# Kernel optimization log

Measured on AMD Instinct MI355X. Metric: run time of the kernel, lower is better.

## Reference

```python
import jax, jax.numpy as jnp
import numpy as np

B, T, C = 4, 2048, 1024
H = 16
D = C // H  # head_dim = 64


def setup_inputs() -> dict:
    key = jax.random.key(0)
    ks = jax.random.split(key, 11)
    s = 0.02
    return {
        "q": jax.random.normal(ks[0], (B, T, C), jnp.float32),
        "k": jax.random.normal(ks[1], (B, T, C), jnp.float32),
        "v": jax.random.normal(ks[2], (B, T, C), jnp.float32),
        "Wq": jax.random.normal(ks[3], (C, C), jnp.float32) * s,
        "bq": jnp.zeros((C,), jnp.float32),
        "Wk": jax.random.normal(ks[4], (C, C), jnp.float32) * s,
        "bk": jnp.zeros((C,), jnp.float32),
        "Wv": jax.random.normal(ks[5], (C, C), jnp.float32) * s,
        "bv": jnp.zeros((C,), jnp.float32),
        "Wo": jax.random.normal(ks[6], (C, C), jnp.float32) * s,
        "bo": jnp.zeros((C,), jnp.float32),
    }


def reference(q, k, v, Wq, bq, Wk, bk, Wv, bv, Wo, bo):
    # projections (torch Linear: x @ W.T + b)
    qh = (q @ Wq.T + bq).reshape(B, T, H, D).transpose(0, 2, 1, 3)  # [B,H,T,D]
    kh = (k @ Wk.T + bk).reshape(B, T, H, D).transpose(0, 2, 1, 3)
    vh = (v @ Wv.T + bv).reshape(B, T, H, D).transpose(0, 2, 1, 3)
    scores = jnp.einsum('bhqd,bhkd->bhqk', qh, kh) * (D ** -0.5)  # [B,H,T,T]
    # causal mask (is_causal=True)
    causal = jnp.tril(jnp.ones((T, T), bool))
    scores = jnp.where(causal, scores, -jnp.inf)
    probs = jax.nn.softmax(scores, axis=-1)
    # dropout_rate=0.0 -> identity in eval mode
    out = jnp.einsum('bhqk,bhkd->bhqd', probs, vh)  # [B,H,T,D]
    out = out.transpose(0, 2, 1, 3).reshape(B, T, C)
    return out @ Wo.T + bo
```

## Files before the change

### kernel.cpp

```cpp
#include <hip/hip_runtime.h>
#include <hip/hip_bf16.h>

typedef __attribute__((ext_vector_type(8))) short bf16x8;
typedef __attribute__((ext_vector_type(4))) float f32x4;
typedef __attribute__((ext_vector_type(16))) float f32x16;

__device__ __forceinline__ unsigned short f2bf(float x) {
  union { float f; unsigned u; } v; v.f = x;
  unsigned r = v.u + 0x7fffu + ((v.u >> 16) & 1u);
  return (unsigned short)(r >> 16);
}

__device__ __forceinline__ unsigned cvtpk_bf16(float lo, float hi) {
  unsigned r;
  asm("v_cvt_pk_bf16_f32 %0, %1, %2" : "=v"(r) : "v"(lo), "v"(hi));
  return r;
}
__device__ __forceinline__ void pl32swap(unsigned &a, unsigned &b) {
  asm volatile("v_permlane32_swap_b32 %0, %1" : "+v"(a), "+v"(b));
}
__device__ __forceinline__ void gload_lds16(const void* g, void* l) {
  __builtin_amdgcn_global_load_lds((const __attribute__((address_space(1))) void*)g,
                                   (__attribute__((address_space(3))) void*)l, 16, 0, 0);
}

#define SWZ(x) ((x) ^ ((((x) >> 7) & 7) << 4))

__global__ __launch_bounds__(256) void cvt_w(
    const float* __restrict__ W0, const float* __restrict__ W1,
    const float* __restrict__ W2, const float* __restrict__ W3,
    unsigned short* __restrict__ o0, unsigned short* __restrict__ o1,
    unsigned short* __restrict__ o2, unsigned short* __restrict__ o3,
    float s0) {
  const int z = blockIdx.y;
  const float* W = (z == 0) ? W0 : (z == 1) ? W1 : (z == 2) ? W2 : W3;
  unsigned short* o = (z == 0) ? o0 : (z == 1) ? o1 : (z == 2) ? o2 : o3;
  const float s = (z == 0) ? s0 : 1.0f;
  const int i = blockIdx.x * 256 + threadIdx.x;
  const float4 x = ((const float4*)W)[i];
  uint2 u;
  u.x = cvtpk_bf16(x.x * s, x.y * s);
  u.y = cvtpk_bf16(x.z * s, x.w * s);
  ((uint2*)o)[i] = u;
}


__global__ __launch_bounds__(256) void proj_gemm3(
    const float* __restrict__ A0, const float* __restrict__ A1, const float* __restrict__ A2,
    const unsigned short* __restrict__ W0b, const unsigned short* __restrict__ W1b,
    const unsigned short* __restrict__ W2b,
    const float* __restrict__ b0, const float* __restrict__ b1, const float* __restrict__ b2,
    unsigned short* __restrict__ o0, unsigned short* __restrict__ o1,
    unsigned short* __restrict__ o2) {
  const int K = 1024;
  const int NK = 32;
  __shared__ __align__(16) unsigned short As[3][4096];
  __shared__ __align__(16) unsigned short Bs[3][4096];
  const int z = blockIdx.z;
  const float* A = (z == 0) ? A0 : (z == 1) ? A1 : A2;
  const unsigned short* Wb = (z == 0) ? W0b : (z == 1) ? W1b : W2b;
  const float* bias = (z == 0) ? b0 : (z == 1) ? b1 : b2;
  unsigned short* out = (z == 0) ? o0 : (z == 1) ? o1 : o2;
  const float bscale = (z == 0) ? 0.125f * 1.4426950408889634f : 1.0f;
  const int vtrans = (z == 2);

  const int tid = threadIdx.x;
  const int row0 = blockIdx.x * 128;
  const int col0 = blockIdx.y * 128;
  const int lane = tid & 63;
  const int w = tid >> 6;
  const int wm = (w >> 1) * 64, wn = (w & 1) * 64;
  const int fr = lane & 15;
  const int g = lane >> 4;
  const int frh = fr >> 1;
  const int gcf = ((fr & 1) * 4 + g) ^ frh;
  const int aoff = wm * 64 + frh * 128 + gcf * 16;
  const int boff = wn * 64 + frh * 128 + gcf * 16;

  const int ar = tid >> 2;
  const int acq = tid & 3;
  const float* asrc0 = &A[(size_t)(row0 + ar) * K + acq * 8];
  const float* asrc1 = asrc0 + (size_t)64 * K;
  const int awr = (ar >> 1) * 128 + ((((ar & 1) * 4 + acq) ^ ((ar >> 1) & 7)) * 16);

  const unsigned short* bsrc[2];
  int bldso[2];
#pragma unroll
  for (int j = 0; j < 2; ++j) {
    const int L = (w * 2 + j) * 64 + lane;
    const int pp = L >> 3, gc = L & 7;
    const int e = gc ^ (pp & 7);
    const int r = pp * 2 + (e >> 2), c = e & 3;
    bsrc[j] = Wb + (size_t)(col0 + r) * K + c * 8;
    bldso[j] = (w * 2 + j) * 1024;
  }

  f32x4 acc[4][4] = {};
  float4 la0[4], la1[4];

#define LOADA(kt, LA)                                        \
  {                                                          \
    const float* s0_ = asrc0 + (kt) * 32;                    \
    const float* s1_ = asrc1 + (kt) * 32;                    \
    LA[0] = *(const float4*)s0_; LA[1] = *(const float4*)(s0_ + 4); \
    LA[2] = *(const float4*)s1_; LA[3] = *(const float4*)(s1_ + 4); \
  }
#define STOREA(buf, LA)                                               \
  {                                                                   \
    uint4 u0_, u1_;                                                   \
    u0_.x = cvtpk_bf16(LA[0].x, LA[0].y); u0_.y = cvtpk_bf16(LA[0].z, LA[0].w); \
    u0_.z = cvtpk_bf16(LA[1].x, LA[1].y); u0_.w = cvtpk_bf16(LA[1].z, LA[1].w); \
    u1_.x = cvtpk_bf16(LA[2].x, LA[2].y); u1_.y = cvtpk_bf16(LA[2].z, LA[2].w); \
    u1_.z = cvtpk_bf16(LA[3].x, LA[3].y); u1_.w = cvtpk_bf16(LA[3].z, LA[3].w); \
    char* base_ = (char*)As[buf];                                     \
    *(uint4*)(base_ + awr) = u0_;                                     \
    *(uint4*)(base_ + awr + 4096) = u1_;                              \
  }
#define STAGEB(buf, kt)                                               \
  {                                                                   \
    gload_lds16(bsrc[0] + (kt) * 32, (char*)Bs[buf] + bldso[0]);      \
    gload_lds16(bsrc[1] + (kt) * 32, (char*)Bs[buf] + bldso[1]);      \
  }
#define COMPUTE(cb)                                                   \
  {                                                                   \
    const char* Ab_ = (const char*)As[cb];                            \
    const char* Bb_ = (const char*)Bs[cb];                            \
    bf16x8 af[4], bfv[4];                                             \
    _Pragma("unroll")                                                 \
    for (int i = 0; i < 4; ++i) {                                     \
      af[i] = *(const bf16x8*)(Ab_ + aoff + i * 1024);                \
      bfv[i] = *(const bf16x8*)(Bb_ + boff + i * 1024);               \
    }                                                                 \
    _Pragma("unroll")                                                 \
    for (int i = 0; i < 4; ++i)                                       \
      _Pragma("unroll")                                               \
      for (int j = 0; j < 4; ++j)                                     \
        acc[i][j] = __builtin_amdgcn_mfma_f32_16x16x32_bf16(af[i], bfv[j], acc[i][j], 0, 0, 0); \
  }

  STAGEB(0, 0); STAGEB(1, 1);
  LOADA(0, la0); LOADA(1, la1);
  STOREA(0, la0);
  asm volatile("s_waitcnt lgkmcnt(0)" ::: "memory");

  int cur = 0;
  for (int kt = 0; kt < NK; kt += 2) {
    if (kt == 0) asm volatile("s_waitcnt vmcnt(0)" ::: "memory");
    else         asm volatile("s_waitcnt vmcnt(6)" ::: "memory");
    __builtin_amdgcn_sched_barrier(0);
    __builtin_amdgcn_s_barrier();
    __builtin_amdgcn_sched_barrier(0);
    {
      const int nx1 = (cur == 2) ? 0 : cur + 1;
      const int nx2 = (nx1 == 2) ? 0 : nx1 + 1;
      if (kt + 2 < NK) { LOADA(kt + 2, la0); STAGEB(nx2, kt + 2); }
      __builtin_amdgcn_sched_barrier(0);
      COMPUTE(cur);
      STOREA(nx1, la1);
      asm volatile("s_waitcnt lgkmcnt(0)" ::: "memory");
      cur = nx1;
    }
    if (kt + 1 == NK - 1) asm volatile("s_waitcnt vmcnt(0)" ::: "memory");
    else                  asm volatile("s_waitcnt vmcnt(6)" ::: "memory");
    __builtin_amdgcn_sched_barrier(0);
    __builtin_amdgcn_s_barrier();
    __builtin_amdgcn_sched_barrier(0);
    {
      const int nx1 = (cur == 2) ? 0 : cur + 1;
      const int nx2 = (nx1 == 2) ? 0 : nx1 + 1;
      if (kt + 3 < NK) { LOADA(kt + 3, la1); STAGEB(nx2, kt + 3); }
      __builtin_amdgcn_sched_barrier(0);
      COMPUTE(cur);
      if (kt + 2 < NK) {
        STOREA(nx1, la0);
        asm volatile("s_waitcnt lgkmcnt(0)" ::: "memory");
      }
      cur = nx1;
    }
  }
#undef LOADA
#undef STOREA
#undef STAGEB
#undef COMPUTE

#pragma unroll
  for (int j = 0; j < 4; ++j) {
    const int n = col0 + wn + j * 16 + fr;
    const float bv = bias[n] * bscale;
    const int h = n >> 6, d = n & 63;
#pragma unroll
    for (int i = 0; i < 4; ++i) {
      const int mrow = row0 + wm + i * 16 + g * 4;
      const int b = mrow >> 11, t0 = mrow & 2047;
      if (vtrans) {
        uint2 u;
        u.x = cvtpk_bf16(acc[i][j][0] + bv, acc[i][j][1] + bv);
        u.y = cvtpk_bf16(acc[i][j][2] + bv, acc[i][j][3] + bv);
        *(uint2*)(&out[(((size_t)b * 16 + h) * 64 + d) * 2048 + t0]) = u;
      } else {
#pragma unroll
        for (int r = 0; r < 4; ++r)
          out[(((size_t)b * 16 + h) * 2048 + (t0 + r)) * 64 + d] = f2bf(acc[i][j][r] + bv);
      }
    }
  }
}

__global__ __launch_bounds__(256) void out_gemm(
    const unsigned short* __restrict__ A, const unsigned short* __restrict__ Wb,
    const float* __restrict__ bias, float* __restrict__ out) {
  const int K = 1024;
  const int NK = 32;
  __shared__ __align__(16) unsigned short As[3][4096];
  __shared__ __align__(16) unsigned short Bs[3][4096];
  const int tid = threadIdx.x;
  const int row0 = blockIdx.x * 128;
  const int col0 = blockIdx.y * 128;
  const int lane = tid & 63;
  const int w = tid >> 6;
  const int wm = (w >> 1) * 64, wn = (w & 1) * 64;
  const int fr = lane & 15;
  const int g = lane >> 4;
  const int frh = fr >> 1;
  const int gcf = ((fr & 1) * 4 + g) ^ frh;
  const int aoff = wm * 64 + frh * 128 + gcf * 16;
  const int boff = wn * 64 + frh * 128 + gcf * 16;

  const unsigned short* asrc[2];
  const unsigned short* bsrc[2];
  int ldso[2];
#pragma unroll
  for (int j = 0; j < 2; ++j) {
    const int L = (w * 2 + j) * 64 + lane;
    const int pp = L >> 3, gc = L & 7;
    const int e = gc ^ (pp & 7);
    const int r = pp * 2 + (e >> 2), c = e & 3;
    asrc[j] = A + (size_t)(row0 + r) * K + c * 8;
    bsrc[j] = Wb + (size_t)(col0 + r) * K + c * 8;
    ldso[j] = (w * 2 + j) * 1024;
  }

  f32x4 acc[4][4] = {};

  auto stage = [&](int buf, int kt) {
#pragma unroll
    for (int j = 0; j < 2; ++j) {
      gload_lds16(asrc[j] + kt * 32, (char*)As[buf] + ldso[j]);
      gload_lds16(bsrc[j] + kt * 32, (char*)Bs[buf] + ldso[j]);
    }
  };

  stage(0, 0); stage(1, 1);
  int cur = 0;
  for (int kt = 0; kt < NK; ++kt) {
    if (kt == 0 || kt == NK - 1) asm volatile("s_waitcnt vmcnt(0)" ::: "memory");
    else                         asm volatile("s_waitcnt vmcnt(4)" ::: "memory");
    __builtin_amdgcn_sched_barrier(0);
    __builtin_amdgcn_s_barrier();
    __builtin_amdgcn_sched_barrier(0);
    const int nx1 = (cur == 2) ? 0 : cur + 1;
    const int nx2 = (nx1 == 2) ? 0 : nx1 + 1;
    if (kt + 2 < NK) stage(nx2, kt + 2);
    __builtin_amdgcn_sched_barrier(0);
    const char* Ab = (const char*)As[cur];
    const char* Bb = (const char*)Bs[cur];
    bf16x8 af[4], bfv[4];
#pragma unroll
    for (int i = 0; i < 4; ++i) {
      af[i] = *(const bf16x8*)(Ab + aoff + i * 1024);
      bfv[i] = *(const bf16x8*)(Bb + boff + i * 1024);
    }
#pragma unroll
    for (int i = 0; i < 4; ++i)
#pragma unroll
      for (int j = 0; j < 4; ++j)
        acc[i][j] = __builtin_amdgcn_mfma_f32_16x16x32_bf16(af[i], bfv[j], acc[i][j], 0, 0, 0);
    cur = nx1;
  }

#pragma unroll
  for (int j = 0; j < 4; ++j) {
    const int n = col0 + wn + j * 16 + fr;
    const float bv = bias[n];
#pragma unroll
    for (int i = 0; i < 4; ++i) {
      const int mrow = row0 + wm + i * 16 + g * 4;
#pragma unroll
      for (int r = 0; r < 4; ++r)
        out[(size_t)(mrow + r) * 1024 + n] = acc[i][j][r] + bv;
    }
  }
}

__global__ __launch_bounds__(256) void attn_mfma(
    const unsigned short* __restrict__ qh, const unsigned short* __restrict__ kh,
    const unsigned short* __restrict__ vT, unsigned short* __restrict__ Ob) {
  __shared__ __align__(16) unsigned short Klds[2][64 * 64];
  __shared__ __align__(16) unsigned short Vlds[2][64 * 64];

  const int tid = threadIdx.x;
  const int lane = tid & 63;
  const int w = tid >> 6;
  const int bh = blockIdx.y;
  const int b = bh >> 4, h = bh & 15;
  const int q32 = lane & 31;
  const int hi = lane >> 5;

  const char* kbase = (const char*)(kh + (size_t)bh * 2048 * 64);
  const char* vbase = (const char*)(vT + (size_t)bh * 64 * 2048);

  const int lrow = lane >> 3;
  const int cb = (((lane & 7) ^ lrow) << 4);

  auto stage = [&](int buf, int t) {
    const int kv0 = t * 64;
#pragma unroll
    for (int j = 0; j < 2; ++j) {
      const int c = w * 2 + j;
      const int r = c * 8 + lrow;
      gload_lds16(kbase + (size_t)(kv0 + r) * 128 + cb,
                  (char*)Klds[buf] + c * 1024);
      gload_lds16(vbase + (size_t)r * 4096 + (size_t)kv0 * 2 + cb,
                  (char*)Vlds[buf] + c * 1024);
    }
  };

  for (int pass = 0; pass < 2; ++pass) {
    const int qt = pass == 0 ? (15 - (int)blockIdx.x) : (int)blockIdx.x;
    const int qb = qt * 128 + w * 32;
    const int nt = 2 * qt + 2;

    bf16x8 qf[4];
    {
      const unsigned short* qp = qh + ((size_t)bh * 2048 + qb + q32) * 64;
#pragma unroll
      for (int kk = 0; kk < 4; ++kk)
        qf[kk] = *(const bf16x8*)(qp + kk * 16 + hi * 8);
    }

    f32x16 acc_o[2] = {};
    float m_run = -INFINITY, l_run = 0.f;

    stage(0, 0);
    __syncthreads();

    int cur = 0;
    for (int t = 0; t < nt; ++t) {
      const int kv0 = t * 64;
      if (t + 1 < nt) stage(cur ^ 1, t + 1);

      if (kv0 < qb + 32) {
        const char* Kb = (const char*)Klds[cur];
        const char* Vb = (const char*)Vlds[cur];

        f32x16 sacc[2] = {};
        __builtin_amdgcn_s_setprio(1);
#pragma unroll
        for (int kk = 0; kk < 4; ++kk) {
          bf16x8 kf0 = *(const bf16x8*)(Kb + SWZ((q32) * 128 + kk * 32 + hi * 16));
          bf16x8 kf1 = *(const bf16x8*)(Kb + SWZ((32 + q32) * 128 + kk * 32 + hi * 16));
          sacc[0] = __builtin_amdgcn_mfma_f32_32x32x16_bf16(kf0, qf[kk], sacc[0], 0, 0, 0);
          sacc[1] = __builtin_amdgcn_mfma_f32_32x32x16_bf16(kf1, qf[kk], sacc[1], 0, 0, 0);
        }
        __builtin_amdgcn_s_setprio(0);

        if (kv0 + 64 > qb) {
          const int qa = qb + q32;
#pragma unroll
          for (int mkv = 0; mkv < 2; ++mkv)
#pragma unroll
            for (int r = 0; r < 16; ++r) {
              const int kva = kv0 + mkv * 32 + 4 * hi + (r & 3) + 8 * (r >> 2);
              if (kva > qa) sacc[mkv][r] = -INFINITY;
            }
        }

        float mx = -INFINITY;
#pragma unroll
        for (int mkv = 0; mkv < 2; ++mkv)
#pragma unroll
          for (int r = 0; r < 16; ++r) mx = fmaxf(mx, sacc[mkv][r]);
        mx = fmaxf(mx, __shfl_xor(mx, 32));
        if (!__all(mx <= m_run + 8.f)) {
          const float mnew = fmaxf(m_run, mx);
          const float al = exp2f(m_run - mnew);
          m_run = mnew;
          l_run *= al;
          acc_o[0] = acc_o[0] * al;
          acc_o[1] = acc_o[1] * al;
        }

        float ls = 0.f;
        unsigned W[2][8];
#pragma unroll
        for (int mkv = 0; mkv < 2; ++mkv)
#pragma unroll
          for (int s = 0; s < 8; ++s) {
            const float p0 = exp2f(sacc[mkv][2 * s] - m_run);
            const float p1 = exp2f(sacc[mkv][2 * s + 1] - m_run);
            ls += p0 + p1;
            W[mkv][s] = cvtpk_bf16(p0, p1);
          }
        ls += __shfl_xor(ls, 32);
        l_run += ls;

#pragma unroll
        for (int mkv = 0; mkv < 2; ++mkv) {
          pl32swap(W[mkv][0], W[mkv][2]);
          pl32swap(W[mkv][1], W[mkv][3]);
          pl32swap(W[mkv][4], W[mkv][6]);
          pl32swap(W[mkv][5], W[mkv][7]);
        }

        __builtin_amdgcn_s_setprio(1);
#pragma unroll
        for (int wg = 0; wg < 4; ++wg) {
          union { unsigned u[4]; bf16x8 v; } pk;
          pk.u[0] = W[wg >> 1][(wg & 1) * 4 + 0];
          pk.u[1] = W[wg >> 1][(wg & 1) * 4 + 1];
          pk.u[2] = W[wg >> 1][(wg & 1) * 4 + 2];
          pk.u[3] = W[wg >> 1][(wg & 1) * 4 + 3];
          bf16x8 vf0 = *(const bf16x8*)(Vb + SWZ((q32) * 128 + wg * 32 + hi * 16));
          bf16x8 vf1 = *(const bf16x8*)(Vb + SWZ((32 + q32) * 128 + wg * 32 + hi * 16));
          acc_o[0] = __builtin_amdgcn_mfma_f32_32x32x16_bf16(vf0, pk.v, acc_o[0], 0, 0, 0);
          acc_o[1] = __builtin_amdgcn_mfma_f32_32x32x16_bf16(vf1, pk.v, acc_o[1], 0, 0, 0);
        }
        __builtin_amdgcn_s_setprio(0);
      }

      __syncthreads();
      cur ^= 1;
    }

    {
      const float inv = 1.0f / l_run;
      const int qa = qb + q32;
      unsigned short* op = Ob + ((size_t)b * 2048 + qa) * 1024 + h * 64;
#pragma unroll
      for (int md = 0; md < 2; ++md)
#pragma unroll
        for (int rr = 0; rr < 4; ++rr) {
          uint2 u;
          u.x = cvtpk_bf16(acc_o[md][rr * 4 + 0] * inv, acc_o[md][rr * 4 + 1] * inv);
          u.y = cvtpk_bf16(acc_o[md][rr * 4 + 2] * inv, acc_o[md][rr * 4 + 3] * inv);
          *(uint2*)(op + md * 32 + rr * 8 + hi * 4) = u;
        }
    }
  }
}

extern "C" void kernel_launch(void* const* d_in, const int* in_sizes, int n_in,
                              void* d_out, int out_size, void* d_ws, size_t ws_size,
                              hipStream_t stream) {
  (void)in_sizes; (void)n_in; (void)out_size; (void)ws_size;
  const float* q = (const float*)d_in[0];
  const float* k = (const float*)d_in[1];
  const float* v = (const float*)d_in[2];
  const float* Wq = (const float*)d_in[3];
  const float* bq = (const float*)d_in[4];
  const float* Wk = (const float*)d_in[5];
  const float* bk = (const float*)d_in[6];
  const float* Wv = (const float*)d_in[7];
  const float* bv = (const float*)d_in[8];
  const float* Wo = (const float*)d_in[9];
  const float* bo = (const float*)d_in[10];
  float* out = (float*)d_out;

  const size_t SZ = (size_t)4 * 16 * 2048 * 64;
  const size_t WSZ = (size_t)1024 * 1024;
  unsigned short* qh = (unsigned short*)d_ws;
  unsigned short* kh = qh + SZ;
  unsigned short* vT = kh + SZ;
  unsigned short* Ob = vT + SZ;
  unsigned short* Wqb = Ob + SZ;
  unsigned short* Wkb = Wqb + WSZ;
  unsigned short* Wvb = Wkb + WSZ;
  unsigned short* Wob = Wvb + WSZ;

  dim3 g0(1024, 4), b0(256);
  cvt_w<<<g0, b0, 0, stream>>>(Wq, Wk, Wv, Wo, Wqb, Wkb, Wvb, Wob,
                               0.125f * 1.4426950408889634f);

  dim3 g1(64, 8, 3), b1(256);
  proj_gemm3<<<g1, b1, 0, stream>>>(q, k, v, Wqb, Wkb, Wvb, bq, bk, bv, qh, kh, vT);

  dim3 g2(8, 64), b2(256);
  attn_mfma<<<g2, b2, 0, stream>>>(qh, kh, vT, Ob);

  dim3 g3(64, 8), b3(256);
  out_gemm<<<g3, b3, 0, stream>>>(Ob, Wob, bo, out);
}
```

Before: 201.2 us.

## Load activation operand straight to registers, stage only weights in LDS

```diff
diff --git a/kernel.cpp b/kernel.cpp
--- a/kernel.cpp
+++ b/kernel.cpp
@@ -54,10 +54,9 @@
     unsigned short* __restrict__ o2) {
   const int K = 1024;
   const int NK = 32;
-  __shared__ __align__(16) unsigned short As[3][4096];
-  __shared__ __align__(16) unsigned short Bs[3][4096];
+  __shared__ __align__(16) unsigned short Ws[3][4096];
   const int z = blockIdx.z;
-  const float* A = (z == 0) ? A0 : (z == 1) ? A1 : A2;
+  const float* X = (z == 0) ? A0 : (z == 1) ? A1 : A2;
   const unsigned short* Wb = (z == 0) ? W0b : (z == 1) ? W1b : W2b;
   const float* bias = (z == 0) ? b0 : (z == 1) ? b1 : b2;
   unsigned short* out = (z == 0) ? o0 : (z == 1) ? o1 : o2;
@@ -65,229 +64,257 @@
   const int vtrans = (z == 2);
 
   const int tid = threadIdx.x;
-  const int row0 = blockIdx.x * 128;
-  const int col0 = blockIdx.y * 128;
+  const int m0 = blockIdx.x * 128;
+  const int n0 = blockIdx.y * 128;
   const int lane = tid & 63;
   const int w = tid >> 6;
-  const int wm = (w >> 1) * 64, wn = (w & 1) * 64;
+  const int wnA = (w >> 1) * 64;
+  const int wmB = (w & 1) * 64;
   const int fr = lane & 15;
   const int g = lane >> 4;
   const int frh = fr >> 1;
   const int gcf = ((fr & 1) * 4 + g) ^ frh;
-  const int aoff = wm * 64 + frh * 128 + gcf * 16;
-  const int boff = wn * 64 + frh * 128 + gcf * 16;
-
-  const int ar = tid >> 2;
-  const int acq = tid & 3;
-  const float* asrc0 = &A[(size_t)(row0 + ar) * K + acq * 8];
-  const float* asrc1 = asrc0 + (size_t)64 * K;
-  const int awr = (ar >> 1) * 128 + ((((ar & 1) * 4 + acq) ^ ((ar >> 1) & 7)) * 16);
-
-  const unsigned short* bsrc[2];
-  int bldso[2];
+  const int aoff = wnA * 64 + frh * 128 + gcf * 16;
+
+  const unsigned short* wsrc[2];
+  int wldo[2];
 #pragma unroll
   for (int j = 0; j < 2; ++j) {
     const int L = (w * 2 + j) * 64 + lane;
     const int pp = L >> 3, gc = L & 7;
     const int e = gc ^ (pp & 7);
     const int r = pp * 2 + (e >> 2), c = e & 3;
-    bsrc[j] = Wb + (size_t)(col0 + r) * K + c * 8;
-    bldso[j] = (w * 2 + j) * 1024;
-  }
+    wsrc[j] = Wb + (size_t)(n0 + r) * K + c * 8;
+    wldo[j] = (w * 2 + j) * 1024;
+  }
+
+  const float* xsrc[4];
+#pragma unroll
+  for (int j = 0; j < 4; ++j)
+    xsrc[j] = X + (size_t)(m0 + wmB + j * 16 + fr) * K + g * 8;
 
   f32x4 acc[4][4] = {};
-  float4 la0[4], la1[4];
-
-#define LOADA(kt, LA)                                        \
-  {                                                          \
-    const float* s0_ = asrc0 + (kt) * 32;                    \
-    const float* s1_ = asrc1 + (kt) * 32;                    \
-    LA[0] = *(const float4*)s0_; LA[1] = *(const float4*)(s0_ + 4); \
-    LA[2] = *(const float4*)s1_; LA[3] = *(const float4*)(s1_ + 4); \
-  }
-#define STOREA(buf, LA)                                               \
+  float4 laA[8], laB[8];
+
+#define LOADX(kt, LA)                                                 \
   {                                                                   \
-    uint4 u0_, u1_;                                                   \
-    u0_.x = cvtpk_bf16(LA[0].x, LA[0].y); u0_.y = cvtpk_bf16(LA[0].z, LA[0].w); \
-    u0_.z = cvtpk_bf16(LA[1].x, LA[1].y); u0_.w = cvtpk_bf16(LA[1].z, LA[1].w); \
-    u1_.x = cvtpk_bf16(LA[2].x, LA[2].y); u1_.y = cvtpk_bf16(LA[2].z, LA[2].w); \
-    u1_.z = cvtpk_bf16(LA[3].x, LA[3].y); u1_.w = cvtpk_bf16(LA[3].z, LA[3].w); \
-    char* base_ = (char*)As[buf];                                     \
-    *(uint4*)(base_ + awr) = u0_;                                     \
-    *(uint4*)(base_ + awr + 4096) = u1_;                              \
-  }
-#define STAGEB(buf, kt)                                               \
+    _Pragma("unroll")                                                 \
+    for (int j = 0; j < 4; ++j) {                                     \
+      LA[j * 2 + 0] = *(const float4*)(xsrc[j] + (kt) * 32);          \
+      LA[j * 2 + 1] = *(const float4*)(xsrc[j] + (kt) * 32 + 4);      \
+    }                                                                 \
+  }
+#define STAGEW(buf, kt)                                               \
   {                                                                   \
-    gload_lds16(bsrc[0] + (kt) * 32, (char*)Bs[buf] + bldso[0]);      \
-    gload_lds16(bsrc[1] + (kt) * 32, (char*)Bs[buf] + bldso[1]);      \
-  }
-#define COMPUTE(cb)                                                   \
+    gload_lds16(wsrc[0] + (kt) * 32, (char*)Ws[buf] + wldo[0]);       \
+    gload_lds16(wsrc[1] + (kt) * 32, (char*)Ws[buf] + wldo[1]);       \
+  }
+#define COMPUTE(cb, LA)                                               \
   {                                                                   \
-    const char* Ab_ = (const char*)As[cb];                            \
-    const char* Bb_ = (const char*)Bs[cb];                            \
-    bf16x8 af[4], bfv[4];                                             \
-    _Pragma("unroll")                                                 \
-    for (int i = 0; i < 4; ++i) {                                     \
-      af[i] = *(const bf16x8*)(Ab_ + aoff + i * 1024);                \
-      bfv[i] = *(const bf16x8*)(Bb_ + boff + i * 1024);               \
+    union { unsigned u[4]; bf16x8 v; } xf[4];                         \
+    _Pragma("unroll")                                                 \
+    for (int j = 0; j < 4; ++j) {                                     \
+      xf[j].u[0] = cvtpk_bf16(LA[j * 2 + 0].x, LA[j * 2 + 0].y);      \
+      xf[j].u[1] = cvtpk_bf16(LA[j * 2 + 0].z, LA[j * 2 + 0].w);      \
+      xf[j].u[2] = cvtpk_bf16(LA[j * 2 + 1].x, LA[j * 2 + 1].y);      \
+      xf[j].u[3] = cvtpk_bf16(LA[j * 2 + 1].z, LA[j * 2 + 1].w);      \
     }                                                                 \
+    const char* Ab_ = (const char*)Ws[cb];                            \
+    bf16x8 af[4];                                                     \
+    _Pragma("unroll")                                                 \
+    for (int i = 0; i < 4; ++i) af[i] = *(const bf16x8*)(Ab_ + aoff + i * 1024); \
     _Pragma("unroll")                                                 \
     for (int i = 0; i < 4; ++i)                                       \
       _Pragma("unroll")                                               \
       for (int j = 0; j < 4; ++j)                                     \
-        acc[i][j] = __builtin_amdgcn_mfma_f32_16x16x32_bf16(af[i], bfv[j], acc[i][j], 0, 0, 0); \
-  }
-
-  STAGEB(0, 0); STAGEB(1, 1);
-  LOADA(0, la0); LOADA(1, la1);
-  STOREA(0, la0);
-  asm volatile("s_waitcnt lgkmcnt(0)" ::: "memory");
+        acc[i][j] = __builtin_amdgcn_mfma_f32_16x16x32_bf16(af[i], xf[j].v, acc[i][j], 0, 0, 0); \
+  }
+
+  LOADX(0, laA);
+  __builtin_amdgcn_sched_barrier(0);
+  STAGEW(0, 0); STAGEW(1, 1);
+  __builtin_amdgcn_sched_barrier(0);
 
   int cur = 0;
   for (int kt = 0; kt < NK; kt += 2) {
-    if (kt == 0) asm volatile("s_waitcnt vmcnt(0)" ::: "memory");
-    else         asm volatile("s_waitcnt vmcnt(6)" ::: "memory");
+    asm volatile("s_waitcnt vmcnt(2)" ::: "memory");
     __builtin_amdgcn_sched_barrier(0);
     __builtin_amdgcn_s_barrier();
     __builtin_amdgcn_sched_barrier(0);
     {
       const int nx1 = (cur == 2) ? 0 : cur + 1;
       const int nx2 = (nx1 == 2) ? 0 : nx1 + 1;
-      if (kt + 2 < NK) { LOADA(kt + 2, la0); STAGEB(nx2, kt + 2); }
-      __builtin_amdgcn_sched_barrier(0);
-      COMPUTE(cur);
-      STOREA(nx1, la1);
-      asm volatile("s_waitcnt lgkmcnt(0)" ::: "memory");
+      if (kt + 1 < NK) LOADX(kt + 1, laB);
+      __builtin_amdgcn_sched_barrier(0);
+      if (kt + 2 < NK) STAGEW(nx2, kt + 2);
+      __builtin_amdgcn_sched_barrier(0);
+      COMPUTE(cur, laA);
       cur = nx1;
     }
     if (kt + 1 == NK - 1) asm volatile("s_waitcnt vmcnt(0)" ::: "memory");
-    else                  asm volatile("s_waitcnt vmcnt(6)" ::: "memory");
+    else                  asm volatile("s_waitcnt vmcnt(2)" ::: "memory");
     __builtin_amdgcn_sched_barrier(0);
     __builtin_amdgcn_s_barrier();
     __builtin_amdgcn_sched_barrier(0);
     {
       const int nx1 = (cur == 2) ? 0 : cur + 1;
       const int nx2 = (nx1 == 2) ? 0 : nx1 + 1;
-      if (kt + 3 < NK) { LOADA(kt + 3, la1); STAGEB(nx2, kt + 3); }
-      __builtin_amdgcn_sched_barrier(0);
-      COMPUTE(cur);
-      if (kt + 2 < NK) {
-        STOREA(nx1, la0);
-        asm volatile("s_waitcnt lgkmcnt(0)" ::: "memory");
+      if (kt + 2 < NK) LOADX(kt + 2, laA);
+      __builtin_amdgcn_sched_barrier(0);
+      if (kt + 3 < NK) STAGEW(nx2, kt + 3);
+      __builtin_amdgcn_sched_barrier(0);
+      COMPUTE(cur, laB);
+      cur = nx1;
+    }
+  }
+#undef LOADX
+#undef STAGEW
+#undef COMPUTE
+
+#pragma unroll
+  for (int i = 0; i < 4; ++i) {
+    const int nb = n0 + wnA + i * 16 + g * 4;
+    const float4 b4 = *(const float4*)&bias[nb];
+    const int h = nb >> 6, d0 = nb & 63;
+#pragma unroll
+    for (int j = 0; j < 4; ++j) {
+      const int m = m0 + wmB + j * 16 + fr;
+      const int b = m >> 11, t = m & 2047;
+      const float v0 = acc[i][j][0] + b4.x * bscale;
+      const float v1 = acc[i][j][1] + b4.y * bscale;
+      const float v2 = acc[i][j][2] + b4.z * bscale;
+      const float v3 = acc[i][j][3] + b4.w * bscale;
+      if (vtrans) {
+        unsigned short* op = &out[(((size_t)b * 16 + h) * 64 + d0) * 2048 + t];
+        op[0] = f2bf(v0); op[2048] = f2bf(v1);
+        op[4096] = f2bf(v2); op[6144] = f2bf(v3);
+      } else {
+        uint2 u;
+        u.x = cvtpk_bf16(v0, v1);
+        u.y = cvtpk_bf16(v2, v3);
+        *(uint2*)(&out[(((size_t)b * 16 + h) * 2048 + t) * 64 + d0]) = u;
       }
-      cur = nx1;
-    }
-  }
-#undef LOADA
-#undef STOREA
-#undef STAGEB
-#undef COMPUTE
-
-#pragma unroll
-  for (int j = 0; j < 4; ++j) {
-    const int n = col0 + wn + j * 16 + fr;
-    const float bv = bias[n] * bscale;
-    const int h = n >> 6, d = n & 63;
-#pragma unroll
-    for (int i = 0; i < 4; ++i) {
-      const int mrow = row0 + wm + i * 16 + g * 4;
-      const int b = mrow >> 11, t0 = mrow & 2047;
-      if (vtrans) {
-        uint2 u;
-        u.x = cvtpk_bf16(acc[i][j][0] + bv, acc[i][j][1] + bv);
-        u.y = cvtpk_bf16(acc[i][j][2] + bv, acc[i][j][3] + bv);
-        *(uint2*)(&out[(((size_t)b * 16 + h) * 64 + d) * 2048 + t0]) = u;
-      } else {
-#pragma unroll
-        for (int r = 0; r < 4; ++r)
-          out[(((size_t)b * 16 + h) * 2048 + (t0 + r)) * 64 + d] = f2bf(acc[i][j][r] + bv);
-      }
     }
   }
 }
 
 __global__ __launch_bounds__(256) void out_gemm(
-    const unsigned short* __restrict__ A, const unsigned short* __restrict__ Wb,
+    const unsigned short* __restrict__ O, const unsigned short* __restrict__ Wb,
     const float* __restrict__ bias, float* __restrict__ out) {
   const int K = 1024;
   const int NK = 32;
-  __shared__ __align__(16) unsigned short As[3][4096];
-  __shared__ __align__(16) unsigned short Bs[3][4096];
+  __shared__ __align__(16) unsigned short Ws[3][4096];
   const int tid = threadIdx.x;
-  const int row0 = blockIdx.x * 128;
-  const int col0 = blockIdx.y * 128;
+  const int m0 = blockIdx.x * 128;
+  const int n0 = blockIdx.y * 128;
   const int lane = tid & 63;
   const int w = tid >> 6;
-  const int wm = (w >> 1) * 64, wn = (w & 1) * 64;
+  const int wnA = (w >> 1) * 64;
+  const int wmB = (w & 1) * 64;
   const int fr = lane & 15;
   const int g = lane >> 4;
   const int frh = fr >> 1;
   const int gcf = ((fr & 1) * 4 + g) ^ frh;
-  const int aoff = wm * 64 + frh * 128 + gcf * 16;
-  const int boff = wn * 64 + frh * 128 + gcf * 16;
-
-  const unsigned short* asrc[2];
-  const unsigned short* bsrc[2];
-  int ldso[2];
+  const int aoff = wnA * 64 + frh * 128 + gcf * 16;
+
+  const unsigned short* wsrc[2];
+  int wldo[2];
 #pragma unroll
   for (int j = 0; j < 2; ++j) {
     const int L = (w * 2 + j) * 64 + lane;
     const int pp = L >> 3, gc = L & 7;
     const int e = gc ^ (pp & 7);
     const int r = pp * 2 + (e >> 2), c = e & 3;
-    asrc[j] = A + (size_t)(row0 + r) * K + c * 8;
-    bsrc[j] = Wb + (size_t)(col0 + r) * K + c * 8;
-    ldso[j] = (w * 2 + j) * 1024;
-  }
+    wsrc[j] = Wb + (size_t)(n0 + r) * K + c * 8;
+    wldo[j] = (w * 2 + j) * 1024;
+  }
+
+  const unsigned short* xsrc[4];
+#pragma unroll
+  for (int j = 0; j < 4; ++j)
+    xsrc[j] = O + (size_t)(m0 + wmB + j * 16 + fr) * K + g * 8;
 
   f32x4 acc[4][4] = {};
-
-  auto stage = [&](int buf, int kt) {
-#pragma unroll
-    for (int j = 0; j < 2; ++j) {
-      gload_lds16(asrc[j] + kt * 32, (char*)As[buf] + ldso[j]);
-      gload_lds16(bsrc[j] + kt * 32, (char*)Bs[buf] + ldso[j]);
-    }
-  };
-
-  stage(0, 0); stage(1, 1);
+  uint4 laA[4], laB[4];
+
+#define LOADX(kt, LA)                                                 \
+  {                                                                   \
+    _Pragma("unroll")                                                 \
+    for (int j = 0; j < 4; ++j)                                       \
+      LA[j] = *(const uint4*)(xsrc[j] + (kt) * 32);                   \
+  }
+#define STAGEW(buf, kt)                                               \
+  {                                                                   \
+    gload_lds16(wsrc[0] + (kt) * 32, (char*)Ws[buf] + wldo[0]);       \
+    gload_lds16(wsrc[1] + (kt) * 32, (char*)Ws[buf] + wldo[1]);       \
+  }
+#define COMPUTE(cb, LA)                                               \
+  {                                                                   \
+    const char* Ab_ = (const char*)Ws[cb];                            \
+    bf16x8 af[4];                                                     \
+    _Pragma("unroll")                                                 \
+    for (int i = 0; i < 4; ++i) af[i] = *(const bf16x8*)(Ab_ + aoff + i * 1024); \
+    _Pragma("unroll")                                                 \
+    for (int i = 0; i < 4; ++i)                                       \
+      _Pragma("unroll")                                               \
+      for (int j = 0; j < 4; ++j)                                     \
+        acc[i][j] = __builtin_amdgcn_mfma_f32_16x16x32_bf16(af[i], *(const bf16x8*)&LA[j], acc[i][j], 0, 0, 0); \
+  }
+
+  LOADX(0, laA);
+  __builtin_amdgcn_sched_barrier(0);
+  STAGEW(0, 0); STAGEW(1, 1);
+  __builtin_amdgcn_sched_barrier(0);
+
   int cur = 0;
-  for (int kt = 0; kt < NK; ++kt) {
-    if (kt == 0 || kt == NK - 1) asm volatile("s_waitcnt vmcnt(0)" ::: "memory");
-    else                         asm volatile("s_waitcnt vmcnt(4)" ::: "memory");
+  for (int kt = 0; kt < NK; kt += 2) {
+    asm volatile("s_waitcnt vmcnt(2)" ::: "memory");
     __builtin_amdgcn_sched_barrier(0);
     __builtin_amdgcn_s_barrier();
     __builtin_amdgcn_sched_barrier(0);
-    const int nx1 = (cur == 2) ? 0 : cur + 1;
-    const int nx2 = (nx1 == 2) ? 0 : nx1 + 1;
-    if (kt + 2 < NK) stage(nx2, kt + 2);
-    __builtin_amdgcn_sched_barrier(0);
-    const char* Ab = (const char*)As[cur];
-    const char* Bb = (const char*)Bs[cur];
-    bf16x8 af[4], bfv[4];
-#pragma unroll
-    for (int i = 0; i < 4; ++i) {
-      af[i] = *(const bf16x8*)(Ab + aoff + i * 1024);
-      bfv[i] = *(const bf16x8*)(Bb + boff + i * 1024);
-    }
-#pragma unroll
-    for (int i = 0; i < 4; ++i)
-#pragma unroll
-      for (int j = 0; j < 4; ++j)
-        acc[i][j] = __builtin_amdgcn_mfma_f32_16x16x32_bf16(af[i], bfv[j], acc[i][j], 0, 0, 0);
-    cur = nx1;
-  }
-
-#pragma unroll
-  for (int j = 0; j < 4; ++j) {
-    const int n = col0 + wn + j * 16 + fr;
-    const float bv = bias[n];
-#pragma unroll
-    for (int i = 0; i < 4; ++i) {
-      const int mrow = row0 + wm + i * 16 + g * 4;
-#pragma unroll
-      for (int r = 0; r < 4; ++r)
-        out[(size_t)(mrow + r) * 1024 + n] = acc[i][j][r] + bv;
+    {
+      const int nx1 = (cur == 2) ? 0 : cur + 1;
+      const int nx2 = (nx1 == 2) ? 0 : nx1 + 1;
+      if (kt + 1 < NK) LOADX(kt + 1, laB);
+      __builtin_amdgcn_sched_barrier(0);
+      if (kt + 2 < NK) STAGEW(nx2, kt + 2);
+      __builtin_amdgcn_sched_barrier(0);
+      COMPUTE(cur, laA);
+      cur = nx1;
+    }
+    if (kt + 1 == NK - 1) asm volatile("s_waitcnt vmcnt(0)" ::: "memory");
+    else                  asm volatile("s_waitcnt vmcnt(2)" ::: "memory");
+    __builtin_amdgcn_sched_barrier(0);
+    __builtin_amdgcn_s_barrier();
+    __builtin_amdgcn_sched_barrier(0);
+    {
+      const int nx1 = (cur == 2) ? 0 : cur + 1;
+      const int nx2 = (nx1 == 2) ? 0 : nx1 + 1;
+      if (kt + 2 < NK) LOADX(kt + 2, laA);
+      __builtin_amdgcn_sched_barrier(0);
+      if (kt + 3 < NK) STAGEW(nx2, kt + 3);
+      __builtin_amdgcn_sched_barrier(0);
+      COMPUTE(cur, laB);
+      cur = nx1;
+    }
+  }
+#undef LOADX
+#undef STAGEW
+#undef COMPUTE
+
+#pragma unroll
+  for (int i = 0; i < 4; ++i) {
+    const int nb = n0 + wnA + i * 16 + g * 4;
+    const float4 b4 = *(const float4*)&bias[nb];
+#pragma unroll
+    for (int j = 0; j < 4; ++j) {
+      const int m = m0 + wmB + j * 16 + fr;
+      float4 v;
+      v.x = acc[i][j][0] + b4.x;
+      v.y = acc[i][j][1] + b4.y;
+      v.z = acc[i][j][2] + b4.z;
+      v.w = acc[i][j][3] + b4.w;
+      *(float4*)&out[(size_t)m * 1024 + nb] = v;
     }
   }
 }
```

Result: slower. 336.7 us (+67.4%).

## Enlarge projection and output GEMM tiles to 256x128 with 512-thread blocks

Applied to the files above, without the earlier changes.

```diff
diff --git a/kernel.cpp b/kernel.cpp
--- a/kernel.cpp
+++ b/kernel.cpp
@@ -45,7 +45,7 @@
 }
 
 
-__global__ __launch_bounds__(256) void proj_gemm3(
+__global__ __launch_bounds__(512, 4) void proj_gemm3(
     const float* __restrict__ A0, const float* __restrict__ A1, const float* __restrict__ A2,
     const unsigned short* __restrict__ W0b, const unsigned short* __restrict__ W1b,
     const unsigned short* __restrict__ W2b,
@@ -54,7 +54,7 @@
     unsigned short* __restrict__ o2) {
   const int K = 1024;
   const int NK = 32;
-  __shared__ __align__(16) unsigned short As[3][4096];
+  __shared__ __align__(16) unsigned short As[3][8192];
   __shared__ __align__(16) unsigned short Bs[3][4096];
   const int z = blockIdx.z;
   const float* A = (z == 0) ? A0 : (z == 1) ? A1 : A2;
@@ -65,11 +65,12 @@
   const int vtrans = (z == 2);
 
   const int tid = threadIdx.x;
-  const int row0 = blockIdx.x * 128;
+  const int row0 = blockIdx.x * 256;
   const int col0 = blockIdx.y * 128;
   const int lane = tid & 63;
   const int w = tid >> 6;
-  const int wm = (w >> 1) * 64, wn = (w & 1) * 64;
+  const int wm = (w >> 1) * 64;
+  const int wn = (w & 1) * 64;
   const int fr = lane & 15;
   const int g = lane >> 4;
   const int frh = fr >> 1;
@@ -80,19 +81,18 @@
   const int ar = tid >> 2;
   const int acq = tid & 3;
   const float* asrc0 = &A[(size_t)(row0 + ar) * K + acq * 8];
-  const float* asrc1 = asrc0 + (size_t)64 * K;
+  const float* asrc1 = asrc0 + (size_t)128 * K;
   const int awr = (ar >> 1) * 128 + ((((ar & 1) * 4 + acq) ^ ((ar >> 1) & 7)) * 16);
 
-  const unsigned short* bsrc[2];
-  int bldso[2];
-#pragma unroll
-  for (int j = 0; j < 2; ++j) {
-    const int L = (w * 2 + j) * 64 + lane;
+  const unsigned short* bsrc;
+  int bldo;
+  {
+    const int L = w * 64 + lane;
     const int pp = L >> 3, gc = L & 7;
     const int e = gc ^ (pp & 7);
     const int r = pp * 2 + (e >> 2), c = e & 3;
-    bsrc[j] = Wb + (size_t)(col0 + r) * K + c * 8;
-    bldso[j] = (w * 2 + j) * 1024;
+    bsrc = Wb + (size_t)(col0 + r) * K + c * 8;
+    bldo = w * 1024;
   }
 
   f32x4 acc[4][4] = {};
@@ -114,13 +114,10 @@
     u1_.z = cvtpk_bf16(LA[3].x, LA[3].y); u1_.w = cvtpk_bf16(LA[3].z, LA[3].w); \
     char* base_ = (char*)As[buf];                                     \
     *(uint4*)(base_ + awr) = u0_;                                     \
-    *(uint4*)(base_ + awr + 4096) = u1_;                              \
+    *(uint4*)(base_ + awr + 8192) = u1_;      \
   }
 #define STAGEB(buf, kt)                                               \
-  {                                                                   \
-    gload_lds16(bsrc[0] + (kt) * 32, (char*)Bs[buf] + bldso[0]);      \
-    gload_lds16(bsrc[1] + (kt) * 32, (char*)Bs[buf] + bldso[1]);      \
-  }
+  { gload_lds16(bsrc + (kt) * 32, (char*)Bs[buf] + bldo); }
 #define COMPUTE(cb)                                                   \
   {                                                                   \
     const char* Ab_ = (const char*)As[cb];                            \
@@ -146,7 +143,7 @@
   int cur = 0;
   for (int kt = 0; kt < NK; kt += 2) {
     if (kt == 0) asm volatile("s_waitcnt vmcnt(0)" ::: "memory");
-    else         asm volatile("s_waitcnt vmcnt(6)" ::: "memory");
+    else         asm volatile("s_waitcnt vmcnt(5)" ::: "memory");
     __builtin_amdgcn_sched_barrier(0);
     __builtin_amdgcn_s_barrier();
     __builtin_amdgcn_sched_barrier(0);
@@ -161,7 +158,7 @@
       cur = nx1;
     }
     if (kt + 1 == NK - 1) asm volatile("s_waitcnt vmcnt(0)" ::: "memory");
-    else                  asm volatile("s_waitcnt vmcnt(6)" ::: "memory");
+    else                  asm volatile("s_waitcnt vmcnt(5)" ::: "memory");
     __builtin_amdgcn_sched_barrier(0);
     __builtin_amdgcn_s_barrier();
     __builtin_amdgcn_sched_barrier(0);
@@ -206,19 +203,20 @@
   }
 }
 
-__global__ __launch_bounds__(256) void out_gemm(
+__global__ __launch_bounds__(512, 4) void out_gemm(
     const unsigned short* __restrict__ A, const unsigned short* __restrict__ Wb,
     const float* __restrict__ bias, float* __restrict__ out) {
   const int K = 1024;
   const int NK = 32;
-  __shared__ __align__(16) unsigned short As[3][4096];
+  __shared__ __align__(16) unsigned short As[3][8192];
   __shared__ __align__(16) unsigned short Bs[3][4096];
   const int tid = threadIdx.x;
-  const int row0 = blockIdx.x * 128;
+  const int row0 = blockIdx.x * 256;
   const int col0 = blockIdx.y * 128;
   const int lane = tid & 63;
   const int w = tid >> 6;
-  const int wm = (w >> 1) * 64, wn = (w & 1) * 64;
+  const int wm = (w >> 1) * 64;
+  const int wn = (w & 1) * 64;
   const int fr = lane & 15;
   const int g = lane >> 4;
   const int frh = fr >> 1;
@@ -227,8 +225,7 @@
   const int boff = wn * 64 + frh * 128 + gcf * 16;
 
   const unsigned short* asrc[2];
-  const unsigned short* bsrc[2];
-  int ldso[2];
+  int aldo[2];
 #pragma unroll
   for (int j = 0; j < 2; ++j) {
     const int L = (w * 2 + j) * 64 + lane;
@@ -236,25 +233,32 @@
     const int e = gc ^ (pp & 7);
     const int r = pp * 2 + (e >> 2), c = e & 3;
     asrc[j] = A + (size_t)(row0 + r) * K + c * 8;
-    bsrc[j] = Wb + (size_t)(col0 + r) * K + c * 8;
-    ldso[j] = (w * 2 + j) * 1024;
+    aldo[j] = (w * 2 + j) * 1024;
+  }
+  const unsigned short* bsrc;
+  int bldo;
+  {
+    const int L = w * 64 + lane;
+    const int pp = L >> 3, gc = L & 7;
+    const int e = gc ^ (pp & 7);
+    const int r = pp * 2 + (e >> 2), c = e & 3;
+    bsrc = Wb + (size_t)(col0 + r) * K + c * 8;
+    bldo = w * 1024;
   }
 
   f32x4 acc[4][4] = {};
 
   auto stage = [&](int buf, int kt) {
-#pragma unroll
-    for (int j = 0; j < 2; ++j) {
-      gload_lds16(asrc[j] + kt * 32, (char*)As[buf] + ldso[j]);
-      gload_lds16(bsrc[j] + kt * 32, (char*)Bs[buf] + ldso[j]);
-    }
+    gload_lds16(asrc[0] + kt * 32, (char*)As[buf] + aldo[0]);
+    gload_lds16(asrc[1] + kt * 32, (char*)As[buf] + aldo[1]);
+    gload_lds16(bsrc + kt * 32, (char*)Bs[buf] + bldo);
   };
 
   stage(0, 0); stage(1, 1);
   int cur = 0;
   for (int kt = 0; kt < NK; ++kt) {
     if (kt == 0 || kt == NK - 1) asm volatile("s_waitcnt vmcnt(0)" ::: "memory");
-    else                         asm volatile("s_waitcnt vmcnt(4)" ::: "memory");
+    else                         asm volatile("s_waitcnt vmcnt(3)" ::: "memory");
     __builtin_amdgcn_sched_barrier(0);
     __builtin_amdgcn_s_barrier();
     __builtin_amdgcn_sched_barrier(0);
@@ -481,12 +485,12 @@
   cvt_w<<<g0, b0, 0, stream>>>(Wq, Wk, Wv, Wo, Wqb, Wkb, Wvb, Wob,
                                0.125f * 1.4426950408889634f);
 
-  dim3 g1(64, 8, 3), b1(256);
+  dim3 g1(32, 8, 3), b1(512);
   proj_gemm3<<<g1, b1, 0, stream>>>(q, k, v, Wqb, Wkb, Wvb, bq, bk, bv, qh, kh, vT);
 
   dim3 g2(8, 64), b2(256);
   attn_mfma<<<g2, b2, 0, stream>>>(qh, kh, vT, Ob);
 
-  dim3 g3(64, 8), b3(256);
+  dim3 g3(32, 8), b3(512);
   out_gemm<<<g3, b3, 0, stream>>>(Ob, Wob, bo, out);
 }
```

After: 289.8 us. 1.44x slower.
